# Kernel optimization log

Hardware: AMD Instinct MI355X
Metric: run time of the kernel (lower is better)

Reference implementation:

```python
import jax, jax.numpy as jnp
import numpy as np

N = 200000    # nodes
DMAX = 32     # max in-degree (padded)
F = 128       # in_feats
H = 128       # lstm hidden == in_feats (use_pp=False)
OUT = 128     # out_feats


def setup_inputs() -> dict:
    key = jax.random.key(0)
    ks = jax.random.split(key, 11)
    u = lambda k, shape, s: jax.random.uniform(k, shape, jnp.float32, -s, s)
    feat = jax.random.normal(ks[0], (N, F), jnp.float32)
    # norms come from sqrt(degree) in the original; keep them positive, O(1)
    in_norm = jax.random.uniform(ks[1], (N,), jnp.float32) + 1.0
    out_norm = jax.random.uniform(ks[2], (N,), jnp.float32) + 1.0
    neighbors = jax.random.randint(ks[3], (N, DMAX), 0, N, jnp.int32)
    degrees = jax.random.randint(ks[4], (N,), 1, DMAX + 1, jnp.int32)
    s_lstm = 1.0 / np.sqrt(H)   # torch LSTM default init scale
    s_lin = 1.0 / np.sqrt(F)    # module's reset_parameters scale
    W_ih = u(ks[5], (4 * H, F), s_lstm)
    W_hh = u(ks[6], (4 * H, H), s_lstm)
    b_ih = u(ks[7], (4 * H,), s_lstm)
    b_hh = u(ks[8], (4 * H,), s_lstm)
    W_lin = u(ks[9], (OUT, F), s_lin)
    b_lin = u(ks[10], (OUT,), s_lin)
    return dict(feat=feat, in_norm=in_norm, out_norm=out_norm,
                W_ih=W_ih, W_hh=W_hh, b_ih=b_ih, b_hh=b_hh,
                W_lin=W_lin, b_lin=b_lin,
                neighbors=neighbors, degrees=degrees)


def reference(feat, in_norm, out_norm, W_ih, W_hh, b_ih, b_hh, W_lin, b_lin,
              neighbors, degrees):
    # graph.nodes['_U'].data['h'] = feat / out_norm
    msg_src = feat / out_norm[:, None]                      # [N, F]
    n, dmax = neighbors.shape
    h_dim = W_hh.shape[1]
    step_mask = jnp.arange(dmax)[None, :] < degrees[:, None]  # [N, DMAX]

    def step(carry, xs):
        h, c = carry
        idx_t, m_t = xs                                      # [N], [N]
        x = msg_src[idx_t]                                   # gather messages [N, F]
        gates = x @ W_ih.T + b_ih + h @ W_hh.T + b_hh        # [N, 4H]
        i, f, g, o = jnp.split(gates, 4, axis=-1)
        i = jax.nn.sigmoid(i)
        f = jax.nn.sigmoid(f)
        o = jax.nn.sigmoid(o)
        g = jnp.tanh(g)
        c_new = f * c + i * g
        h_new = o * jnp.tanh(c_new)
        m = m_t[:, None]
        return (jnp.where(m, h_new, h), jnp.where(m, c_new, c)), None

    init = (jnp.zeros((n, h_dim), feat.dtype), jnp.zeros((n, h_dim), feat.dtype))
    (h_final, _), _ = jax.lax.scan(step, init, (neighbors.T, step_mask.T))
    # feat = linear(h / in_norm)
    return (h_final / in_norm[:, None]) @ W_lin.T + b_lin
```

## Files before the change

### kernel.cpp

```cpp
#include <hip/hip_runtime.h>

#define NN 200000
#define NB 64
#define NWG (NN / NB)

typedef unsigned short u16;
typedef unsigned int u32;
typedef __attribute__((ext_vector_type(8))) short short8;
typedef __attribute__((ext_vector_type(4))) float f32x4;

__device__ __forceinline__ u16 f2bf(float x) {
  u32 u = __float_as_uint(x);
  u += 0x7FFFu + ((u >> 16) & 1u);
  return (u16)(u >> 16);
}
__device__ __forceinline__ float sigf(float x) {
  float e = __builtin_amdgcn_exp2f(x * -1.44269504f);
  return __builtin_amdgcn_rcpf(1.0f + e);
}
__device__ __forceinline__ float tanhf_(float x) {
  float e = __builtin_amdgcn_exp2f(x * 2.88539008f);
  return 1.0f - 2.0f * __builtin_amdgcn_rcpf(1.0f + e);
}

__global__ void k_prep_msg(const float* __restrict__ feat, const float* __restrict__ onorm,
                           u16* __restrict__ msg) {
  int i = blockIdx.x * 256 + threadIdx.x;
  int row = i >> 4, c8 = (i & 15) * 8;
  const float4 a = *(const float4*)(feat + (size_t)row * 128 + c8);
  const float4 b = *(const float4*)(feat + (size_t)row * 128 + c8 + 4);
  float s = 1.0f / onorm[row];
  short8 v = { (short)f2bf(a.x * s), (short)f2bf(a.y * s), (short)f2bf(a.z * s), (short)f2bf(a.w * s),
               (short)f2bf(b.x * s), (short)f2bf(b.y * s), (short)f2bf(b.z * s), (short)f2bf(b.w * s) };
  *(short8*)(msg + (size_t)row * 128 + c8) = v;
}

__global__ void k_prep_w(const float* __restrict__ Wih, const float* __restrict__ Whh,
                         const float* __restrict__ Wlin, const float* __restrict__ bih,
                         const float* __restrict__ bhh, u16* __restrict__ wihb,
                         u16* __restrict__ whhb, u16* __restrict__ wlinb,
                         float* __restrict__ bsum) {
  int i = blockIdx.x * 256 + threadIdx.x;
  if (i < 65536) wihb[i] = f2bf(Wih[i]);
  else if (i < 131072) whhb[i - 65536] = f2bf(Whh[i - 65536]);
  else if (i < 147456) wlinb[i - 131072] = f2bf(Wlin[i - 131072]);
  else { int j = i - 147456; bsum[j] = bih[j] + bhh[j]; }
}

__global__ void k_hist(const int* __restrict__ degs, int* __restrict__ hist, int n) {
  __shared__ int lh[33];
  if (threadIdx.x < 33) lh[threadIdx.x] = 0;
  __syncthreads();
  int i = blockIdx.x * 256 + threadIdx.x;
  if (i < n) atomicAdd(&lh[degs[i]], 1);
  __syncthreads();
  if (threadIdx.x < 33 && lh[threadIdx.x]) atomicAdd(&hist[threadIdx.x], lh[threadIdx.x]);
}

__global__ void k_scan(const int* __restrict__ hist, int* __restrict__ basep) {
  if (threadIdx.x == 0 && blockIdx.x == 0) {
    int a = 0;
    for (int d = 32; d >= 1; --d) { basep[d] = a; a += hist[d]; }
    basep[0] = a;
  }
}

__global__ void k_scatter(const int* __restrict__ degs, int* __restrict__ basep,
                          int* __restrict__ perm, int n) {
  __shared__ int lh[33], lbase[33], lc[33];
  int t = threadIdx.x;
  if (t < 33) { lh[t] = 0; lc[t] = 0; }
  __syncthreads();
  int i = blockIdx.x * 256 + t;
  int d = (i < n) ? degs[i] : 0;
  if (i < n) atomicAdd(&lh[d], 1);
  __syncthreads();
  if (t < 33 && lh[t]) lbase[t] = atomicAdd(&basep[t], lh[t]);
  __syncthreads();
  if (i < n) { int r = atomicAdd(&lc[d], 1); perm[lbase[d] + r] = i; }
}

__global__ __launch_bounds__(512, 2) void k_main(
    const u16* __restrict__ msg, const u16* __restrict__ wihb,
    const u16* __restrict__ whhb, const u16* __restrict__ wlinb,
    const float* __restrict__ bsum, const float* __restrict__ blin,
    const float* __restrict__ inorm, const int* __restrict__ nbrs,
    const int* __restrict__ degs, const int* __restrict__ perm,
    float* __restrict__ out) {
  __shared__ alignas(16) u16 Xb[2][64 * 136];
  __shared__ alignas(16) u16 Hb[2][64 * 136];
  __shared__ int nbrl[64 * 33];
  __shared__ int gidl[64];

  const int tid = threadIdx.x;
  const int w = tid >> 6;
  const int lane = tid & 63;
  const int l15 = lane & 15;
  const int g4 = lane >> 4;
  const int w16 = w * 16;
  const int gr = tid >> 4;
  const int gc = (tid & 15) * 8;
  const int base = blockIdx.x * NB;

  if (tid < NB) gidl[tid] = perm[base + tid];
  __syncthreads();

#pragma unroll
  for (int s = 0; s < 4; ++s) {
    int i = tid + s * 512;
    nbrl[(i >> 5) * 33 + (i & 31)] = nbrs[(size_t)gidl[i >> 5] * 32 + (i & 31)];
  }
  {
    u32* hz = (u32*)Hb[0];
#pragma unroll
    for (int s = 0; s < 8; ++s) hz[tid + s * 512] = 0;
    if (tid < 256) hz[tid + 4096] = 0;
  }
  short8 fih[4][4], fhh[4][4];
#pragma unroll
  for (int g = 0; g < 4; ++g)
#pragma unroll
    for (int kk = 0; kk < 4; ++kk) {
      size_t o = (size_t)(g * 128 + w16 + l15) * 128 + kk * 32 + g4 * 8;
      fih[g][kk] = *(const short8*)(wihb + o);
      fhh[g][kk] = *(const short8*)(whhb + o);
    }
  float bias[4];
#pragma unroll
  for (int g = 0; g < 4; ++g) bias[g] = bsum[g * 128 + w16 + l15];

  u32 dgp[4];
#pragma unroll
  for (int r = 0; r < 4; ++r) {
    u32 p = 0;
#pragma unroll
    for (int q = 0; q < 4; ++q) p |= ((u32)degs[gidl[r * 16 + g4 * 4 + q]]) << (8 * q);
    dgp[r] = p;
  }
  const int maxdeg = degs[gidl[0]];

  float c[4][4] = {};
  u16 hbf[4][4] = {};
  __syncthreads();

  short8 pf0, pf1;
  {
    int n0 = nbrl[gr * 33], n1 = nbrl[(gr + 32) * 33];
    pf0 = *(const short8*)(msg + (size_t)n0 * 128 + gc);
    pf1 = *(const short8*)(msg + (size_t)n1 * 128 + gc);
  }
  *(short8*)(&Xb[0][gr * 136 + gc]) = pf0;
  *(short8*)(&Xb[0][(gr + 32) * 136 + gc]) = pf1;
  __syncthreads();

  for (int t = 0; t < maxdeg; ++t) {
    const int cur = t & 1, nxt = cur ^ 1;
    if (t + 1 < maxdeg) {
      int n0 = nbrl[gr * 33 + t + 1], n1 = nbrl[(gr + 32) * 33 + t + 1];
      pf0 = *(const short8*)(msg + (size_t)n0 * 128 + gc);
      pf1 = *(const short8*)(msg + (size_t)n1 * 128 + gc);
    }
#pragma unroll
    for (int rp = 0; rp < 2; ++rp) {
      f32x4 acc[2][4];
#pragma unroll
      for (int r = 0; r < 2; ++r)
#pragma unroll
        for (int g = 0; g < 4; ++g) acc[r][g] = (f32x4){bias[g], bias[g], bias[g], bias[g]};
#pragma unroll
      for (int kk = 0; kk < 4; ++kk) {
        short8 ax0 = *(const short8*)(&Xb[cur][(rp * 32 + l15) * 136 + kk * 32 + g4 * 8]);
        short8 ax1 = *(const short8*)(&Xb[cur][(rp * 32 + 16 + l15) * 136 + kk * 32 + g4 * 8]);
        short8 ah0 = *(const short8*)(&Hb[cur][(rp * 32 + l15) * 136 + kk * 32 + g4 * 8]);
        short8 ah1 = *(const short8*)(&Hb[cur][(rp * 32 + 16 + l15) * 136 + kk * 32 + g4 * 8]);
#pragma unroll
        for (int g = 0; g < 4; ++g) {
          acc[0][g] = __builtin_amdgcn_mfma_f32_16x16x32_bf16(ax0, fih[g][kk], acc[0][g], 0, 0, 0);
          acc[0][g] = __builtin_amdgcn_mfma_f32_16x16x32_bf16(ah0, fhh[g][kk], acc[0][g], 0, 0, 0);
          acc[1][g] = __builtin_amdgcn_mfma_f32_16x16x32_bf16(ax1, fih[g][kk], acc[1][g], 0, 0, 0);
          acc[1][g] = __builtin_amdgcn_mfma_f32_16x16x32_bf16(ah1, fhh[g][kk], acc[1][g], 0, 0, 0);
        }
      }
#pragma unroll
      for (int r = 0; r < 2; ++r) {
        const int rr = rp * 2 + r;
#pragma unroll
        for (int q = 0; q < 4; ++q) {
          float iv = sigf(acc[r][0][q]);
          float fv = sigf(acc[r][1][q]);
          float gv = tanhf_(acc[r][2][q]);
          float ov = sigf(acc[r][3][q]);
          float cn = fv * c[rr][q] + iv * gv;
          float hn = ov * tanhf_(cn);
          bool act = (int)((dgp[rr] >> (8 * q)) & 255u) > t;
          c[rr][q] = act ? cn : c[rr][q];
          hbf[rr][q] = act ? f2bf(hn) : hbf[rr][q];
        }
      }
    }
    if (t + 1 < maxdeg) {
      *(short8*)(&Xb[nxt][gr * 136 + gc]) = pf0;
      *(short8*)(&Xb[nxt][(gr + 32) * 136 + gc]) = pf1;
    }
#pragma unroll
    for (int rr = 0; rr < 4; ++rr)
#pragma unroll
      for (int q = 0; q < 4; ++q)
        Hb[nxt][(rr * 16 + g4 * 4 + q) * 136 + w16 + l15] = hbf[rr][q];
    __syncthreads();
  }

  const u16* Hf = Hb[maxdeg & 1];

  short8 wl[4];
#pragma unroll
  for (int kk = 0; kk < 4; ++kk)
    wl[kk] = *(const short8*)(wlinb + (size_t)(w16 + l15) * 128 + kk * 32 + g4 * 8);
  f32x4 a2[4] = {};
#pragma unroll
  for (int kk = 0; kk < 4; ++kk)
#pragma unroll
    for (int r = 0; r < 4; ++r) {
      short8 ah = *(const short8*)(&Hf[(r * 16 + l15) * 136 + kk * 32 + g4 * 8]);
      a2[r] = __builtin_amdgcn_mfma_f32_16x16x32_bf16(ah, wl[kk], a2[r], 0, 0, 0);
    }
  float blv = blin[w16 + l15];
#pragma unroll
  for (int r = 0; r < 4; ++r)
#pragma unroll
    for (int q = 0; q < 4; ++q) {
      int nl = r * 16 + g4 * 4 + q;
      int g = gidl[nl];
      out[(size_t)g * 128 + w16 + l15] = a2[r][q] / inorm[g] + blv;
    }
}

extern "C" void kernel_launch(void* const* d_in, const int* in_sizes, int n_in,
                              void* d_out, int out_size, void* d_ws, size_t ws_size,
                              hipStream_t stream) {
  const float* feat    = (const float*)d_in[0];
  const float* in_norm = (const float*)d_in[1];
  const float* out_nrm = (const float*)d_in[2];
  const float* W_ih    = (const float*)d_in[3];
  const float* W_hh    = (const float*)d_in[4];
  const float* b_ih    = (const float*)d_in[5];
  const float* b_hh    = (const float*)d_in[6];
  const float* W_lin   = (const float*)d_in[7];
  const float* b_lin   = (const float*)d_in[8];
  const int* neighbors = (const int*)d_in[9];
  const int* degrees   = (const int*)d_in[10];
  float* out = (float*)d_out;

  char* ws = (char*)d_ws;
  u16* msg    = (u16*)(ws);
  u16* wihb   = (u16*)(ws + 51200000);
  u16* whhb   = (u16*)(ws + 51331072);
  u16* wlinb  = (u16*)(ws + 51462144);
  float* bsum = (float*)(ws + 51494912);
  int* perm   = (int*)(ws + 51496960);
  int* hist   = (int*)(ws + 52296960);
  int* basep  = hist + 64;
  if (ws_size < 52297600) return;

  hipMemsetAsync(hist, 0, 64 * 4, stream);
  k_prep_msg<<<12500, 256, 0, stream>>>(feat, out_nrm, msg);
  k_prep_w<<<578, 256, 0, stream>>>(W_ih, W_hh, W_lin, b_ih, b_hh, wihb, whhb, wlinb, bsum);
  k_hist<<<782, 256, 0, stream>>>(degrees, hist, NN);
  k_scan<<<1, 1, 0, stream>>>(hist, basep);
  k_scatter<<<782, 256, 0, stream>>>(degrees, basep, perm, NN);
  k_main<<<NWG, 512, 0, stream>>>(msg, wihb, whhb, wlinb, bsum, b_lin, in_norm,
                                  neighbors, degrees, perm, out);
}
```

Baseline: 1.167 ms.

## Prescale gate weights, split x/h MFMAs across barrier, drop LDS neighbor table

Folds the -log2e and 2*log2e factors of sigmoid and tanh into the bf16 gate weights and bias during prep. The cell then calls exp2 directly and merges the reciprocals into fewer rcp calls. The input-projection MFMAs for the next step now run right after the barrier into a 64-wide accumulator, so only the recurrent h-MFMAs sit on the critical path before the nonlinearity. Neighbor indices are read from global memory two steps ahead instead of being staged in an LDS table, and the message gather is issued after the LDS writes. The cost is higher register pressure from 16 live accumulators, and rounding the prescaled weights to bf16 may shift numerics slightly.

Result: slower. 2.074 ms (+77.7%).

```diff
diff --git a/kernel.cpp b/kernel.cpp
--- a/kernel.cpp
+++ b/kernel.cpp
@@ -9,18 +9,13 @@
 typedef __attribute__((ext_vector_type(8))) short short8;
 typedef __attribute__((ext_vector_type(4))) float f32x4;
 
+#define LOG2E 1.4426950408889634f
+#define TWOLOG2E 2.8853900817779268f
+
 __device__ __forceinline__ u16 f2bf(float x) {
   u32 u = __float_as_uint(x);
   u += 0x7FFFu + ((u >> 16) & 1u);
   return (u16)(u >> 16);
-}
-__device__ __forceinline__ float sigf(float x) {
-  float e = __builtin_amdgcn_exp2f(x * -1.44269504f);
-  return __builtin_amdgcn_rcpf(1.0f + e);
-}
-__device__ __forceinline__ float tanhf_(float x) {
-  float e = __builtin_amdgcn_exp2f(x * 2.88539008f);
-  return 1.0f - 2.0f * __builtin_amdgcn_rcpf(1.0f + e);
 }
 
 __global__ void k_prep_msg(const float* __restrict__ feat, const float* __restrict__ onorm,
@@ -41,10 +36,22 @@
                          u16* __restrict__ whhb, u16* __restrict__ wlinb,
                          float* __restrict__ bsum) {
   int i = blockIdx.x * 256 + threadIdx.x;
-  if (i < 65536) wihb[i] = f2bf(Wih[i]);
-  else if (i < 131072) whhb[i - 65536] = f2bf(Whh[i - 65536]);
-  else if (i < 147456) wlinb[i - 131072] = f2bf(Wlin[i - 131072]);
-  else { int j = i - 147456; bsum[j] = bih[j] + bhh[j]; }
+  if (i < 65536) {
+    int gate = (i >> 7) >> 7;
+    float s = (gate == 2) ? TWOLOG2E : -LOG2E;
+    wihb[i] = f2bf(Wih[i] * s);
+  } else if (i < 131072) {
+    int j = i - 65536;
+    int gate = (j >> 7) >> 7;
+    float s = (gate == 2) ? TWOLOG2E : -LOG2E;
+    whhb[j] = f2bf(Whh[j] * s);
+  } else if (i < 147456) {
+    wlinb[i - 131072] = f2bf(Wlin[i - 131072]);
+  } else {
+    int j = i - 147456;
+    float s = ((j >> 7) == 2) ? TWOLOG2E : -LOG2E;
+    bsum[j] = (bih[j] + bhh[j]) * s;
+  }
 }
 
 __global__ void k_hist(const int* __restrict__ degs, int* __restrict__ hist, int n) {
@@ -87,9 +94,8 @@
     const float* __restrict__ inorm, const int* __restrict__ nbrs,
     const int* __restrict__ degs, const int* __restrict__ perm,
     float* __restrict__ out) {
-  __shared__ alignas(16) u16 Xb[2][64 * 136];
-  __shared__ alignas(16) u16 Hb[2][64 * 136];
-  __shared__ int nbrl[64 * 33];
+  __shared__ alignas(16) u16 Xl[2][64 * 136];
+  __shared__ alignas(16) u16 Hl[2][64 * 136];
   __shared__ int gidl[64];
 
   const int tid = threadIdx.x;
@@ -103,19 +109,16 @@
   const int base = blockIdx.x * NB;
 
   if (tid < NB) gidl[tid] = perm[base + tid];
-  __syncthreads();
-
-#pragma unroll
-  for (int s = 0; s < 4; ++s) {
-    int i = tid + s * 512;
-    nbrl[(i >> 5) * 33 + (i & 31)] = nbrs[(size_t)gidl[i >> 5] * 32 + (i & 31)];
-  }
   {
-    u32* hz = (u32*)Hb[0];
+    u32* hz = (u32*)Hl[0];
 #pragma unroll
     for (int s = 0; s < 8; ++s) hz[tid + s * 512] = 0;
     if (tid < 256) hz[tid + 4096] = 0;
   }
+  __syncthreads();
+
+  const int gid0 = gidl[gr], gid1 = gidl[gr + 32];
+
   short8 fih[4][4], fhh[4][4];
 #pragma unroll
   for (int g = 0; g < 4; ++g)
@@ -139,78 +142,133 @@
   }
   const int maxdeg = degs[gidl[0]];
 
+  {
+    int i0 = nbrs[(size_t)gid0 * 32], i1 = nbrs[(size_t)gid1 * 32];
+    short8 p0 = *(const short8*)(msg + (size_t)i0 * 128 + gc);
+    short8 p1 = *(const short8*)(msg + (size_t)i1 * 128 + gc);
+    *(short8*)(&Xl[0][gr * 136 + gc]) = p0;
+    *(short8*)(&Xl[0][(gr + 32) * 136 + gc]) = p1;
+  }
   float c[4][4] = {};
   u16 hbf[4][4] = {};
   __syncthreads();
 
+  f32x4 Xacc[4][4];
+#pragma unroll
+  for (int r = 0; r < 4; ++r)
+#pragma unroll
+    for (int g = 0; g < 4; ++g) Xacc[r][g] = (f32x4){bias[g], bias[g], bias[g], bias[g]};
+#pragma unroll
+  for (int kk = 0; kk < 4; ++kk) {
+    short8 a0 = *(const short8*)(&Xl[0][(l15) * 136 + kk * 32 + g4 * 8]);
+    short8 a1 = *(const short8*)(&Xl[0][(16 + l15) * 136 + kk * 32 + g4 * 8]);
+    short8 a2 = *(const short8*)(&Xl[0][(32 + l15) * 136 + kk * 32 + g4 * 8]);
+    short8 a3 = *(const short8*)(&Xl[0][(48 + l15) * 136 + kk * 32 + g4 * 8]);
+#pragma unroll
+    for (int g = 0; g < 4; ++g) {
+      Xacc[0][g] = __builtin_amdgcn_mfma_f32_16x16x32_bf16(a0, fih[g][kk], Xacc[0][g], 0, 0, 0);
+      Xacc[1][g] = __builtin_amdgcn_mfma_f32_16x16x32_bf16(a1, fih[g][kk], Xacc[1][g], 0, 0, 0);
+      Xacc[2][g] = __builtin_amdgcn_mfma_f32_16x16x32_bf16(a2, fih[g][kk], Xacc[2][g], 0, 0, 0);
+      Xacc[3][g] = __builtin_amdgcn_mfma_f32_16x16x32_bf16(a3, fih[g][kk], Xacc[3][g], 0, 0, 0);
+    }
+  }
+
   short8 pf0, pf1;
-  {
-    int n0 = nbrl[gr * 33], n1 = nbrl[(gr + 32) * 33];
-    pf0 = *(const short8*)(msg + (size_t)n0 * 128 + gc);
-    pf1 = *(const short8*)(msg + (size_t)n1 * 128 + gc);
-  }
-  *(short8*)(&Xb[0][gr * 136 + gc]) = pf0;
-  *(short8*)(&Xb[0][(gr + 32) * 136 + gc]) = pf1;
-  __syncthreads();
-
+  if (maxdeg > 1) {
+    int i0 = nbrs[(size_t)gid0 * 32 + 1], i1 = nbrs[(size_t)gid1 * 32 + 1];
+    pf0 = *(const short8*)(msg + (size_t)i0 * 128 + gc);
+    pf1 = *(const short8*)(msg + (size_t)i1 * 128 + gc);
+  }
+
+  int cur = 0;
   for (int t = 0; t < maxdeg; ++t) {
-    const int cur = t & 1, nxt = cur ^ 1;
-    if (t + 1 < maxdeg) {
-      int n0 = nbrl[gr * 33 + t + 1], n1 = nbrl[(gr + 32) * 33 + t + 1];
-      pf0 = *(const short8*)(msg + (size_t)n0 * 128 + gc);
-      pf1 = *(const short8*)(msg + (size_t)n1 * 128 + gc);
-    }
-#pragma unroll
-    for (int rp = 0; rp < 2; ++rp) {
-      f32x4 acc[2][4];
-#pragma unroll
-      for (int r = 0; r < 2; ++r)
-#pragma unroll
-        for (int g = 0; g < 4; ++g) acc[r][g] = (f32x4){bias[g], bias[g], bias[g], bias[g]};
+    const int nxt = cur ^ 1;
+    int ni0 = 0, ni1 = 0;
+    if (t + 2 < maxdeg) {
+      ni0 = nbrs[(size_t)gid0 * 32 + t + 2];
+      ni1 = nbrs[(size_t)gid1 * 32 + t + 2];
+    }
+
+    {
+      const u16* Hc = &Hl[cur][0];
 #pragma unroll
       for (int kk = 0; kk < 4; ++kk) {
-        short8 ax0 = *(const short8*)(&Xb[cur][(rp * 32 + l15) * 136 + kk * 32 + g4 * 8]);
-        short8 ax1 = *(const short8*)(&Xb[cur][(rp * 32 + 16 + l15) * 136 + kk * 32 + g4 * 8]);
-        short8 ah0 = *(const short8*)(&Hb[cur][(rp * 32 + l15) * 136 + kk * 32 + g4 * 8]);
-        short8 ah1 = *(const short8*)(&Hb[cur][(rp * 32 + 16 + l15) * 136 + kk * 32 + g4 * 8]);
+        short8 a0 = *(const short8*)(&Hc[(l15) * 136 + kk * 32 + g4 * 8]);
+        short8 a1 = *(const short8*)(&Hc[(16 + l15) * 136 + kk * 32 + g4 * 8]);
+        short8 a2 = *(const short8*)(&Hc[(32 + l15) * 136 + kk * 32 + g4 * 8]);
+        short8 a3 = *(const short8*)(&Hc[(48 + l15) * 136 + kk * 32 + g4 * 8]);
 #pragma unroll
         for (int g = 0; g < 4; ++g) {
-          acc[0][g] = __builtin_amdgcn_mfma_f32_16x16x32_bf16(ax0, fih[g][kk], acc[0][g], 0, 0, 0);
-          acc[0][g] = __builtin_amdgcn_mfma_f32_16x16x32_bf16(ah0, fhh[g][kk], acc[0][g], 0, 0, 0);
-          acc[1][g] = __builtin_amdgcn_mfma_f32_16x16x32_bf16(ax1, fih[g][kk], acc[1][g], 0, 0, 0);
-          acc[1][g] = __builtin_amdgcn_mfma_f32_16x16x32_bf16(ah1, fhh[g][kk], acc[1][g], 0, 0, 0);
+          Xacc[0][g] = __builtin_amdgcn_mfma_f32_16x16x32_bf16(a0, fhh[g][kk], Xacc[0][g], 0, 0, 0);
+          Xacc[1][g] = __builtin_amdgcn_mfma_f32_16x16x32_bf16(a1, fhh[g][kk], Xacc[1][g], 0, 0, 0);
+          Xacc[2][g] = __builtin_amdgcn_mfma_f32_16x16x32_bf16(a2, fhh[g][kk], Xacc[2][g], 0, 0, 0);
+          Xacc[3][g] = __builtin_amdgcn_mfma_f32_16x16x32_bf16(a3, fhh[g][kk], Xacc[3][g], 0, 0, 0);
         }
       }
-#pragma unroll
-      for (int r = 0; r < 2; ++r) {
-        const int rr = rp * 2 + r;
-#pragma unroll
-        for (int q = 0; q < 4; ++q) {
-          float iv = sigf(acc[r][0][q]);
-          float fv = sigf(acc[r][1][q]);
-          float gv = tanhf_(acc[r][2][q]);
-          float ov = sigf(acc[r][3][q]);
-          float cn = fv * c[rr][q] + iv * gv;
-          float hn = ov * tanhf_(cn);
-          bool act = (int)((dgp[rr] >> (8 * q)) & 255u) > t;
-          c[rr][q] = act ? cn : c[rr][q];
-          hbf[rr][q] = act ? f2bf(hn) : hbf[rr][q];
+    }
+
+#pragma unroll
+    for (int r = 0; r < 4; ++r)
+#pragma unroll
+      for (int q = 0; q < 4; ++q) {
+        float ei = __builtin_amdgcn_exp2f(Xacc[r][0][q]);
+        float ef = __builtin_amdgcn_exp2f(Xacc[r][1][q]);
+        float eg = __builtin_amdgcn_exp2f(Xacc[r][2][q]);
+        float eo = __builtin_amdgcn_exp2f(Xacc[r][3][q]);
+        float fv  = __builtin_amdgcn_rcpf(1.0f + ef);
+        float rig = __builtin_amdgcn_rcpf((1.0f + ei) * (1.0f + eg));
+        float ig  = (eg - 1.0f) * rig;
+        float cn  = fv * c[r][q] + ig;
+        float ec  = __builtin_amdgcn_exp2f(cn * TWOLOG2E);
+        float rho = __builtin_amdgcn_rcpf((1.0f + eo) * (1.0f + ec));
+        float hn  = (ec - 1.0f) * rho;
+        bool act = (int)((dgp[r] >> (8 * q)) & 255u) > t;
+        c[r][q] = act ? cn : c[r][q];
+        hbf[r][q] = act ? f2bf(hn) : hbf[r][q];
+      }
+
+    if (t + 1 < maxdeg) {
+      *(short8*)(&Xl[nxt][gr * 136 + gc]) = pf0;
+      *(short8*)(&Xl[nxt][(gr + 32) * 136 + gc]) = pf1;
+    }
+#pragma unroll
+    for (int r = 0; r < 4; ++r)
+#pragma unroll
+      for (int q = 0; q < 4; ++q)
+        Hl[nxt][(r * 16 + g4 * 4 + q) * 136 + w16 + l15] = hbf[r][q];
+
+    if (t + 2 < maxdeg) {
+      pf0 = *(const short8*)(msg + (size_t)ni0 * 128 + gc);
+      pf1 = *(const short8*)(msg + (size_t)ni1 * 128 + gc);
+    }
+
+    __syncthreads();
+
+    if (t + 1 < maxdeg) {
+      const u16* Xc = &Xl[nxt][0];
+#pragma unroll
+      for (int r = 0; r < 4; ++r)
+#pragma unroll
+        for (int g = 0; g < 4; ++g) Xacc[r][g] = (f32x4){bias[g], bias[g], bias[g], bias[g]};
+#pragma unroll
+      for (int kk = 0; kk < 4; ++kk) {
+        short8 a0 = *(const short8*)(&Xc[(l15) * 136 + kk * 32 + g4 * 8]);
+        short8 a1 = *(const short8*)(&Xc[(16 + l15) * 136 + kk * 32 + g4 * 8]);
+        short8 a2 = *(const short8*)(&Xc[(32 + l15) * 136 + kk * 32 + g4 * 8]);
+        short8 a3 = *(const short8*)(&Xc[(48 + l15) * 136 + kk * 32 + g4 * 8]);
+#pragma unroll
+        for (int g = 0; g < 4; ++g) {
+          Xacc[0][g] = __builtin_amdgcn_mfma_f32_16x16x32_bf16(a0, fih[g][kk], Xacc[0][g], 0, 0, 0);
+          Xacc[1][g] = __builtin_amdgcn_mfma_f32_16x16x32_bf16(a1, fih[g][kk], Xacc[1][g], 0, 0, 0);
+          Xacc[2][g] = __builtin_amdgcn_mfma_f32_16x16x32_bf16(a2, fih[g][kk], Xacc[2][g], 0, 0, 0);
+          Xacc[3][g] = __builtin_amdgcn_mfma_f32_16x16x32_bf16(a3, fih[g][kk], Xacc[3][g], 0, 0, 0);
         }
       }
     }
-    if (t + 1 < maxdeg) {
-      *(short8*)(&Xb[nxt][gr * 136 + gc]) = pf0;
-      *(short8*)(&Xb[nxt][(gr + 32) * 136 + gc]) = pf1;
-    }
-#pragma unroll
-    for (int rr = 0; rr < 4; ++rr)
-#pragma unroll
-      for (int q = 0; q < 4; ++q)
-        Hb[nxt][(rr * 16 + g4 * 4 + q) * 136 + w16 + l15] = hbf[rr][q];
-    __syncthreads();
-  }
-
-  const u16* Hf = Hb[maxdeg & 1];
+    cur = nxt;
+  }
+
+  const u16* Hf = &Hl[cur][0];
 
   short8 wl[4];
 #pragma unroll
```
